# Kernel tuning notes

Measured on AMD Instinct MI355X. Metric: run time of the kernel, lower is better.

The kernel has to match this reference:

```python
import jax, jax.numpy as jnp
import numpy as np

N, E, FEAT, EMB, HID, V, EA, G = 10000, 250000, 16, 32, 32, 12, 9, 64
TEMP = 1.0


def setup_inputs() -> dict:
    key = jax.random.key(0)
    ks = jax.random.split(key, 20)
    p = lambda k, shp: jax.random.normal(k, shp, dtype=jnp.float32) * 0.05
    return {
        "x": jax.random.normal(ks[0], (N, FEAT), dtype=jnp.float32),
        "edge_attr": jax.random.normal(ks[1], (E, EA), dtype=jnp.float32),
        "edge_index": jax.random.randint(ks[2], (2, E), 0, N),
        "batch": jnp.sort(jax.random.randint(ks[3], (N,), 0, G)),
        # conv1 edge MLP: Linear(EA,32) -> ReLU -> Linear(32, FEAT*EMB)
        "nn1_w1": p(ks[4], (EA, 32)), "nn1_b1": p(ks[5], (32,)),
        "nn1_w2": p(ks[6], (32, FEAT * EMB)), "nn1_b2": p(ks[7], (FEAT * EMB,)),
        "root1": p(ks[8], (FEAT, EMB)), "bias1": p(ks[9], (EMB,)),
        # conv2 edge MLP: Linear(EA,32) -> ReLU -> Linear(32, EMB*HID)
        "nn2_w1": p(ks[10], (EA, 32)), "nn2_b1": p(ks[11], (32,)),
        "nn2_w2": p(ks[12], (32, EMB * HID)), "nn2_b2": p(ks[13], (EMB * HID,)),
        "root2": p(ks[14], (EMB, HID)), "bias2": p(ks[15], (HID,)),
        "lin_w": p(ks[16], (HID, V)), "lin_b": p(ks[17], (V,)),
    }


def _segment_mean(vals, ids, num_segments):
    s = jax.ops.segment_sum(vals, ids, num_segments=num_segments)
    cnt = jax.ops.segment_sum(jnp.ones((vals.shape[0],), vals.dtype), ids,
                              num_segments=num_segments)
    return s / jnp.maximum(cnt, 1.0)[:, None]


def _nnconv(h, edge_attr, src, dst, w1, b1, w2, b2, root, bias, din, dout):
    # edge MLP -> per-edge weight matrix [E, din, dout]
    we = (jax.nn.relu(edge_attr @ w1 + b1) @ w2 + b2).reshape(-1, din, dout)
    msg = jnp.einsum('ei,eio->eo', h[src], we)      # gather + per-edge matmul
    agg = _segment_mean(msg, dst, h.shape[0])       # scatter-mean to targets
    return agg + h @ root + bias                    # root weight + bias


def reference(x, edge_attr, edge_index, batch,
              nn1_w1, nn1_b1, nn1_w2, nn1_b2, root1, bias1,
              nn2_w1, nn2_b1, nn2_w2, nn2_b2, root2, bias2,
              lin_w, lin_b):
    src, dst = edge_index[0], edge_index[1]
    h = jax.nn.relu(_nnconv(x, edge_attr, src, dst,
                            nn1_w1, nn1_b1, nn1_w2, nn1_b2, root1, bias1,
                            FEAT, EMB))
    h = jax.nn.relu(_nnconv(h, edge_attr, src, dst,
                            nn2_w1, nn2_b1, nn2_w2, nn2_b2, root2, bias2,
                            EMB, HID))
    pooled = _segment_mean(h, batch, G)             # global_mean_pool [G, HID]
    logits = (pooled @ lin_w + lin_b) / TEMP
    return jax.nn.log_softmax(logits, axis=1)
```

## Files before the change

### kernel.cpp

```cpp
#include <hip/hip_runtime.h>
#include <hip/hip_bf16.h>
#include <stdint.h>

#define NN 10000
#define NE 250000
#define FEAT 16
#define EMB 32
#define HID 32
#define NV 12
#define EAD 9
#define NG 64
#define EPB 128
#define NCH 25

__device__ __forceinline__ uint32_t bf16rne(float f) {
    uint32_t u = __float_as_uint(f);
    return (u + 0x7fffu + ((u >> 16) & 1u)) >> 16;
}
__device__ __forceinline__ float blo(uint32_t p) { return __uint_as_float(p << 16); }
__device__ __forceinline__ float bhi(uint32_t p) { return __uint_as_float(p & 0xffff0000u); }

__global__ void edge_stats_kernel(const int* __restrict__ src,
                                  const int* __restrict__ dst,
                                  int* __restrict__ histS,
                                  int* __restrict__ histD) {
    int e = blockIdx.x * blockDim.x + threadIdx.x;
    if (e >= NE) return;
    atomicAdd(&histS[src[e]], 1);
    atomicAdd(&histD[dst[e]], 1);
}

__global__ __launch_bounds__(1024) void scan_kernel(const int* __restrict__ hist,
                                                    int* __restrict__ rowStart,
                                                    int* __restrict__ cursor) {
    __shared__ int part[1024];
    int t = threadIdx.x;
    int base = t * 10;
    int local[10];
    int s = 0;
#pragma unroll
    for (int i = 0; i < 10; ++i) {
        int v = (base + i < NN) ? hist[base + i] : 0;
        local[i] = s;
        s += v;
    }
    part[t] = s;
    __syncthreads();
    for (int off = 1; off < 1024; off <<= 1) {
        int v = (t >= off) ? part[t - off] : 0;
        __syncthreads();
        part[t] += v;
        __syncthreads();
    }
    int pre = (t == 0) ? 0 : part[t - 1];
#pragma unroll
    for (int i = 0; i < 10; ++i) {
        if (base + i < NN) {
            int rs = pre + local[i];
            rowStart[base + i] = rs;
            cursor[base + i] = rs;
        }
    }
    if (t == 1023) rowStart[NN] = part[1023];
}

__global__ void scatter_kernel(const float* __restrict__ ea,
                               const int* __restrict__ src,
                               const int* __restrict__ dst,
                               int* __restrict__ cursorS,
                               float* __restrict__ ea_p,
                               int* __restrict__ src_s,
                               int* __restrict__ dst_s) {
    int e = blockIdx.x * blockDim.x + threadIdx.x;
    if (e >= NE) return;
    int sv = src[e];
    int pos = atomicAdd(&cursorS[sv], 1);
    src_s[pos] = sv;
    dst_s[pos] = dst[e];
#pragma unroll
    for (int j = 0; j < 12; ++j)
        ea_p[(size_t)pos * 12 + j] = (j < EAD) ? ea[(size_t)e * EAD + j] : 0.f;
}

template <int DIN>
__global__ __launch_bounds__(256) void computeQ_pack_kernel(
    const float* __restrict__ h,
    const float* __restrict__ w2,
    const float* __restrict__ b2,
    uint32_t* __restrict__ Qp,
    float* __restrict__ Qb)
{
    int t = threadIdx.x;
    int o = t & 31;
    int kk = (blockIdx.y * 256 + t) >> 5;
    float w0[DIN], w1r[DIN];
    const float* wa = w2 + (size_t)(2 * kk) * (DIN * 32) + o;
    const float* wb = w2 + (size_t)(2 * kk + 1) * (DIN * 32) + o;
#pragma unroll
    for (int i = 0; i < DIN; ++i) { w0[i] = wa[i * 32]; w1r[i] = wb[i * 32]; }

    int n0 = blockIdx.x * NCH;
    for (int j = 0; j < NCH; ++j) {
        int n = n0 + j;
        const float* hn = h + (size_t)n * DIN;
        float s0 = 0.f, s1 = 0.f;
#pragma unroll
        for (int i = 0; i < DIN; ++i) {
            float hv = hn[i];
            s0 += hv * w0[i];
            s1 += hv * w1r[i];
        }
        Qp[((size_t)n * 16 + kk) * 32 + o] = (bf16rne(s1) << 16) | bf16rne(s0);
        if (kk == 0) {
            float sb = 0.f;
#pragma unroll
            for (int i = 0; i < DIN; ++i) sb += hn[i] * b2[i * 32 + o];
            Qb[(size_t)n * 32 + o] = sb;
        }
    }
}

__global__ __launch_bounds__(256) void edge_agg_kernel(
    const float* __restrict__ ea_p,
    const int* __restrict__ src_s,
    const int* __restrict__ dst_s,
    const float* __restrict__ w1,
    const float* __restrict__ b1,
    const uint32_t* __restrict__ Qp,
    const float* __restrict__ Qb,
    float* __restrict__ agg)
{
    __shared__ float s_hid[8][32];
    int t = threadIdx.x;
    int o = t & 31;
    int slot = t >> 5;

    float w1r[12];
#pragma unroll
    for (int j = 0; j < 12; ++j) w1r[j] = (j < EAD) ? w1[j * 32 + o] : 0.f;
    float b1r = b1[o];

    int base = blockIdx.x * EPB;
    int eend = min(base + EPB, NE);
    for (int e = base + slot; e < eend; e += 8) {
        const float4* eav = (const float4*)(ea_p + (size_t)e * 12);
        float4 a0 = eav[0], a1 = eav[1], a2 = eav[2];
        float hs = b1r;
        hs += a0.x * w1r[0] + a0.y * w1r[1] + a0.z * w1r[2] + a0.w * w1r[3];
        hs += a1.x * w1r[4] + a1.y * w1r[5] + a1.z * w1r[6] + a1.w * w1r[7];
        hs += a2.x * w1r[8];
        float hd = fmaxf(hs, 0.f);

        s_hid[slot][o] = hd;
        __builtin_amdgcn_wave_barrier();

        int sv = src_s[e];
        const uint32_t* q = Qp + (size_t)sv * 512 + o;
        float m = Qb[(size_t)sv * 32 + o];
        const float4* hq = (const float4*)(&s_hid[slot][0]);
#pragma unroll
        for (int c = 0; c < 8; ++c) {
            float4 hv = hq[c];
            uint32_t qa  = q[(2 * c) * 32];
            uint32_t qb2 = q[(2 * c + 1) * 32];
            m += hv.x * blo(qa) + hv.y * bhi(qa)
               + hv.z * blo(qb2) + hv.w * bhi(qb2);
        }
        atomicAdd(&agg[(size_t)dst_s[e] * 32 + o], m);
        __builtin_amdgcn_wave_barrier();
    }
}

template <int DIN>
__global__ __launch_bounds__(256) void node_update_kernel(
    float* __restrict__ agg,
    const int* __restrict__ histD,
    const float* __restrict__ hin,
    const float* __restrict__ root,
    const float* __restrict__ bias,
    float* __restrict__ hout,
    float* __restrict__ pooled,
    const int* __restrict__ batch,
    float* __restrict__ gcnt)
{
    __shared__ float s_root[DIN][32];
    __shared__ float s_h[32][DIN + 1];
    int t = threadIdx.x;
    int n0 = blockIdx.x * 32;

    for (int i = t; i < DIN * 8; i += 256)
        ((float4*)&s_root[0][0])[i] = ((const float4*)root)[i];
    for (int idx = t; idx < 32 * DIN; idx += 256) {
        int nl = idx / DIN, i = idx - nl * DIN;
        int n = n0 + nl;
        s_h[nl][i] = (n < NN) ? hin[(size_t)n * DIN + i] : 0.f;
    }
    __syncthreads();

    int nl = t >> 3;
    int cg = t & 7;
    int n = n0 + nl;
    if (n >= NN) return;

    float inv = 1.0f / fmaxf((float)histD[n], 1.0f);
    float* ap = agg + (size_t)n * 32 + cg * 4;
    float4 a4;
    a4.x = atomicAdd(ap + 0, 0.f);
    a4.y = atomicAdd(ap + 1, 0.f);
    a4.z = atomicAdd(ap + 2, 0.f);
    a4.w = atomicAdd(ap + 3, 0.f);
    *(float4*)ap = make_float4(0.f, 0.f, 0.f, 0.f);

    float4 b4 = *(const float4*)(bias + cg * 4);
    float4 s;
    s.x = a4.x * inv + b4.x;
    s.y = a4.y * inv + b4.y;
    s.z = a4.z * inv + b4.z;
    s.w = a4.w * inv + b4.w;
#pragma unroll
    for (int i = 0; i < DIN; ++i) {
        float hv = s_h[nl][i];
        float4 r4 = *(const float4*)&s_root[i][cg * 4];
        s.x += hv * r4.x; s.y += hv * r4.y; s.z += hv * r4.z; s.w += hv * r4.w;
    }
    s.x = fmaxf(s.x, 0.f); s.y = fmaxf(s.y, 0.f);
    s.z = fmaxf(s.z, 0.f); s.w = fmaxf(s.w, 0.f);
    *(float4*)(hout + (size_t)n * 32 + cg * 4) = s;

    if (pooled) {
        int g = batch[n];
        atomicAdd(&pooled[g * 32 + cg * 4 + 0], s.x);
        atomicAdd(&pooled[g * 32 + cg * 4 + 1], s.y);
        atomicAdd(&pooled[g * 32 + cg * 4 + 2], s.z);
        atomicAdd(&pooled[g * 32 + cg * 4 + 3], s.w);
        if (cg == 0) atomicAdd(&gcnt[g], 1.0f);
    }
}

__global__ void final_kernel(float* __restrict__ pooled,
                             float* __restrict__ gcnt,
                             const float* __restrict__ lin_w,
                             const float* __restrict__ lin_b,
                             float* __restrict__ out) {
    int g = threadIdx.x;
    if (g >= NG) return;
    float inv = 1.0f / fmaxf(atomicAdd(&gcnt[g], 0.f), 1.0f);
    float p[HID];
#pragma unroll
    for (int h = 0; h < HID; ++h) p[h] = atomicAdd(&pooled[g * HID + h], 0.f) * inv;
    float logits[NV];
    float mx = -1e30f;
#pragma unroll
    for (int v = 0; v < NV; ++v) {
        float s = lin_b[v];
#pragma unroll
        for (int h = 0; h < HID; ++h) s += p[h] * lin_w[h * NV + v];
        logits[v] = s;
        mx = fmaxf(mx, s);
    }
    float se = 0.f;
#pragma unroll
    for (int v = 0; v < NV; ++v) se += expf(logits[v] - mx);
    float lse = mx + logf(se);
#pragma unroll
    for (int v = 0; v < NV; ++v) out[g * NV + v] = logits[v] - lse;
}

extern "C" void kernel_launch(void* const* d_in, const int* in_sizes, int n_in,
                              void* d_out, int out_size, void* d_ws, size_t ws_size,
                              hipStream_t stream) {
    const float* x        = (const float*)d_in[0];
    const float* ea       = (const float*)d_in[1];
    const int*   eidx     = (const int*)d_in[2];
    const int*   batch    = (const int*)d_in[3];
    const float* nn1_w1   = (const float*)d_in[4];
    const float* nn1_b1   = (const float*)d_in[5];
    const float* nn1_w2   = (const float*)d_in[6];
    const float* nn1_b2   = (const float*)d_in[7];
    const float* root1    = (const float*)d_in[8];
    const float* bias1    = (const float*)d_in[9];
    const float* nn2_w1   = (const float*)d_in[10];
    const float* nn2_b1   = (const float*)d_in[11];
    const float* nn2_w2   = (const float*)d_in[12];
    const float* nn2_b2   = (const float*)d_in[13];
    const float* root2    = (const float*)d_in[14];
    const float* bias2    = (const float*)d_in[15];
    const float* lin_w    = (const float*)d_in[16];
    const float* lin_b    = (const float*)d_in[17];
    float* out = (float*)d_out;

    const int* src = eidx;
    const int* dst = eidx + NE;

    char* base = (char*)d_ws;
    uint32_t* Qp   = (uint32_t*)base;
    float* ea_p    = (float*)(Qp + (size_t)NN * 512);
    float* Qb      = ea_p + (size_t)NE * 12;
    float* h1      = Qb + (size_t)NN * 32;
    float* h2      = h1 + (size_t)NN * 32;
    float* agg     = h2 + (size_t)NN * 32;
    int*   src_s   = (int*)(agg + (size_t)NN * 32);
    int*   dst_s   = src_s + NE;
    int*   rowS    = dst_s + NE;
    int*   curS    = rowS + NN + 1;
    int*   histS   = curS + NN;
    int*   histD   = histS + NN;
    float* pooled  = (float*)(histD + NN);
    float* gcnt    = pooled + NG * 32;
    size_t zero_bytes = ((size_t)NN * 2 + NG * 32 + NG) * 4;

    hipMemsetAsync(agg, 0, (size_t)NN * 32 * sizeof(float), stream);
    hipMemsetAsync(histS, 0, zero_bytes, stream);

    edge_stats_kernel<<<(NE + 255) / 256, 256, 0, stream>>>(src, dst, histS, histD);
    scan_kernel<<<1, 1024, 0, stream>>>(histS, rowS, curS);
    scatter_kernel<<<(NE + 255) / 256, 256, 0, stream>>>(ea, src, dst, curS,
                                                         ea_p, src_s, dst_s);

    const int edge_grid = (NE + EPB - 1) / EPB;
    const int node_grid = (NN + 31) / 32;
    dim3 qgrid(NN / NCH, 2);

    computeQ_pack_kernel<FEAT><<<qgrid, 256, 0, stream>>>(x, nn1_w2, nn1_b2, Qp, Qb);
    edge_agg_kernel<<<edge_grid, 256, 0, stream>>>(ea_p, src_s, dst_s,
                                                   nn1_w1, nn1_b1, Qp, Qb, agg);
    node_update_kernel<FEAT><<<node_grid, 256, 0, stream>>>(
        agg, histD, x, root1, bias1, h1, nullptr, nullptr, nullptr);

    computeQ_pack_kernel<EMB><<<qgrid, 256, 0, stream>>>(h1, nn2_w2, nn2_b2, Qp, Qb);
    edge_agg_kernel<<<edge_grid, 256, 0, stream>>>(ea_p, src_s, dst_s,
                                                   nn2_w1, nn2_b1, Qp, Qb, agg);
    node_update_kernel<EMB><<<node_grid, 256, 0, stream>>>(
        agg, histD, h1, root2, bias2, h2, pooled, batch, gcnt);

    final_kernel<<<1, 64, 0, stream>>>(pooled, gcnt, lin_w, lin_b, out);
}
```

Baseline: 262.8 us.

## Fuse per-layer kernels into one cooperative persistent kernel with grid syncs

```diff
diff --git a/kernel.cpp b/kernel.cpp
--- a/kernel.cpp
+++ b/kernel.cpp
@@ -1,6 +1,9 @@
 #include <hip/hip_runtime.h>
 #include <hip/hip_bf16.h>
+#include <hip/hip_cooperative_groups.h>
 #include <stdint.h>
+
+namespace cg = cooperative_groups;
 
 #define NN 10000
 #define NE 250000
@@ -82,172 +85,184 @@
         ea_p[(size_t)pos * 12 + j] = (j < EAD) ? ea[(size_t)e * EAD + j] : 0.f;
 }
 
+struct Params {
+    const float* x; const float* ea_p;
+    const int* src_s; const int* dst_s; const int* histD; const int* batch;
+    const float* nn1_w1; const float* nn1_b1; const float* nn1_w2; const float* nn1_b2;
+    const float* root1; const float* bias1;
+    const float* nn2_w1; const float* nn2_b1; const float* nn2_w2; const float* nn2_b2;
+    const float* root2; const float* bias2;
+    const float* lin_w; const float* lin_b;
+    uint32_t* Qp; float* Qb; float* agg; float* h1; float* h2;
+    float* pooled; float* gcnt; float* out;
+};
+
 template <int DIN>
-__global__ __launch_bounds__(256) void computeQ_pack_kernel(
-    const float* __restrict__ h,
-    const float* __restrict__ w2,
-    const float* __restrict__ b2,
-    uint32_t* __restrict__ Qp,
-    float* __restrict__ Qb)
-{
+__device__ void computeQ_phase(const float* __restrict__ h,
+                               const float* __restrict__ w2,
+                               const float* __restrict__ b2,
+                               uint32_t* __restrict__ Qp,
+                               float* __restrict__ Qb,
+                               float* smem) {
     int t = threadIdx.x;
     int o = t & 31;
-    int kk = (blockIdx.y * 256 + t) >> 5;
-    float w0[DIN], w1r[DIN];
-    const float* wa = w2 + (size_t)(2 * kk) * (DIN * 32) + o;
-    const float* wb = w2 + (size_t)(2 * kk + 1) * (DIN * 32) + o;
-#pragma unroll
-    for (int i = 0; i < DIN; ++i) { w0[i] = wa[i * 32]; w1r[i] = wb[i * 32]; }
-
-    int n0 = blockIdx.x * NCH;
-    for (int j = 0; j < NCH; ++j) {
-        int n = n0 + j;
-        const float* hn = h + (size_t)n * DIN;
-        float s0 = 0.f, s1 = 0.f;
-#pragma unroll
-        for (int i = 0; i < DIN; ++i) {
-            float hv = hn[i];
-            s0 += hv * w0[i];
-            s1 += hv * w1r[i];
-        }
-        Qp[((size_t)n * 16 + kk) * 32 + o] = (bf16rne(s1) << 16) | bf16rne(s0);
-        if (kk == 0) {
-            float sb = 0.f;
-#pragma unroll
-            for (int i = 0; i < DIN; ++i) sb += hn[i] * b2[i * 32 + o];
-            Qb[(size_t)n * 32 + o] = sb;
-        }
-    }
-}
-
-__global__ __launch_bounds__(256) void edge_agg_kernel(
-    const float* __restrict__ ea_p,
-    const int* __restrict__ src_s,
-    const int* __restrict__ dst_s,
-    const float* __restrict__ w1,
-    const float* __restrict__ b1,
-    const uint32_t* __restrict__ Qp,
-    const float* __restrict__ Qb,
-    float* __restrict__ agg)
-{
-    __shared__ float s_hid[8][32];
+    const int NVB = (NN / NCH) * 2;
+    for (int vb = blockIdx.x; vb < NVB; vb += gridDim.x) {
+        int nb = vb >> 1;
+        int kk = (vb & 1) * 8 + (t >> 5);
+        int n0 = nb * NCH;
+        __syncthreads();
+        for (int idx = t; idx < NCH * DIN; idx += 256)
+            smem[idx] = h[(size_t)n0 * DIN + idx];
+        __syncthreads();
+        float w0[DIN], w1r[DIN];
+        const float* wa = w2 + (size_t)(2 * kk) * (DIN * 32) + o;
+        const float* wb = w2 + (size_t)(2 * kk + 1) * (DIN * 32) + o;
+#pragma unroll
+        for (int i = 0; i < DIN; ++i) { w0[i] = wa[i * 32]; w1r[i] = wb[i * 32]; }
+        for (int j = 0; j < NCH; ++j) {
+            const float* sh = smem + j * DIN;
+            float s0 = 0.f, s1 = 0.f;
+#pragma unroll
+            for (int i4 = 0; i4 < DIN / 4; ++i4) {
+                float4 hv = *(const float4*)(sh + i4 * 4);
+                s0 += hv.x * w0[4*i4] + hv.y * w0[4*i4+1] + hv.z * w0[4*i4+2] + hv.w * w0[4*i4+3];
+                s1 += hv.x * w1r[4*i4] + hv.y * w1r[4*i4+1] + hv.z * w1r[4*i4+2] + hv.w * w1r[4*i4+3];
+            }
+            int n = n0 + j;
+            Qp[((size_t)n * 16 + kk) * 32 + o] = (bf16rne(s1) << 16) | bf16rne(s0);
+            if (kk == 0) {
+                float sb = 0.f;
+#pragma unroll
+                for (int i = 0; i < DIN; ++i) sb += sh[i] * b2[i * 32 + o];
+                Qb[(size_t)n * 32 + o] = sb;
+            }
+        }
+    }
+}
+
+__device__ void edge_phase(const float* __restrict__ ea_p,
+                           const int* __restrict__ src_s,
+                           const int* __restrict__ dst_s,
+                           const float* __restrict__ w1,
+                           const float* __restrict__ b1,
+                           const uint32_t* __restrict__ Qp,
+                           const float* __restrict__ Qb,
+                           float* __restrict__ agg,
+                           float* smem) {
+    float* s_hid = smem;
     int t = threadIdx.x;
     int o = t & 31;
     int slot = t >> 5;
-
-    float w1r[12];
-#pragma unroll
-    for (int j = 0; j < 12; ++j) w1r[j] = (j < EAD) ? w1[j * 32 + o] : 0.f;
+    float w1r[EAD];
+#pragma unroll
+    for (int j = 0; j < EAD; ++j) w1r[j] = w1[j * 32 + o];
     float b1r = b1[o];
 
-    int base = blockIdx.x * EPB;
-    int eend = min(base + EPB, NE);
-    for (int e = base + slot; e < eend; e += 8) {
-        const float4* eav = (const float4*)(ea_p + (size_t)e * 12);
-        float4 a0 = eav[0], a1 = eav[1], a2 = eav[2];
-        float hs = b1r;
-        hs += a0.x * w1r[0] + a0.y * w1r[1] + a0.z * w1r[2] + a0.w * w1r[3];
-        hs += a1.x * w1r[4] + a1.y * w1r[5] + a1.z * w1r[6] + a1.w * w1r[7];
-        hs += a2.x * w1r[8];
-        float hd = fmaxf(hs, 0.f);
-
-        s_hid[slot][o] = hd;
-        __builtin_amdgcn_wave_barrier();
-
-        int sv = src_s[e];
-        const uint32_t* q = Qp + (size_t)sv * 512 + o;
-        float m = Qb[(size_t)sv * 32 + o];
-        const float4* hq = (const float4*)(&s_hid[slot][0]);
-#pragma unroll
-        for (int c = 0; c < 8; ++c) {
-            float4 hv = hq[c];
-            uint32_t qa  = q[(2 * c) * 32];
-            uint32_t qb2 = q[(2 * c + 1) * 32];
-            m += hv.x * blo(qa) + hv.y * bhi(qa)
-               + hv.z * blo(qb2) + hv.w * bhi(qb2);
-        }
-        atomicAdd(&agg[(size_t)dst_s[e] * 32 + o], m);
-        __builtin_amdgcn_wave_barrier();
-    }
-}
-
-template <int DIN>
-__global__ __launch_bounds__(256) void node_update_kernel(
-    float* __restrict__ agg,
-    const int* __restrict__ histD,
-    const float* __restrict__ hin,
-    const float* __restrict__ root,
-    const float* __restrict__ bias,
-    float* __restrict__ hout,
-    float* __restrict__ pooled,
-    const int* __restrict__ batch,
-    float* __restrict__ gcnt)
-{
-    __shared__ float s_root[DIN][32];
-    __shared__ float s_h[32][DIN + 1];
+    const int NCHK = (NE + EPB - 1) / EPB;
+    for (int vb = blockIdx.x; vb < NCHK; vb += gridDim.x) {
+        int base = vb * EPB, eend = min(base + EPB, NE);
+        for (int e = base + slot; e < eend; e += 8) {
+            const float4* eav = (const float4*)(ea_p + (size_t)e * 12);
+            float4 a0 = eav[0], a1 = eav[1], a2 = eav[2];
+            float hs = b1r;
+            hs += a0.x * w1r[0] + a0.y * w1r[1] + a0.z * w1r[2] + a0.w * w1r[3];
+            hs += a1.x * w1r[4] + a1.y * w1r[5] + a1.z * w1r[6] + a1.w * w1r[7];
+            hs += a2.x * w1r[8];
+            float hd = fmaxf(hs, 0.f);
+
+            s_hid[slot * 32 + o] = hd;
+            __builtin_amdgcn_wave_barrier();
+
+            int sv = src_s[e];
+            const uint32_t* q = Qp + (size_t)sv * 512 + o;
+            float m = Qb[(size_t)sv * 32 + o];
+            const float4* hq = (const float4*)(s_hid + slot * 32);
+#pragma unroll
+            for (int c = 0; c < 8; ++c) {
+                float4 hv = hq[c];
+                uint32_t qa  = q[(2 * c) * 32];
+                uint32_t qb2 = q[(2 * c + 1) * 32];
+                m += hv.x * blo(qa) + hv.y * bhi(qa)
+                   + hv.z * blo(qb2) + hv.w * bhi(qb2);
+            }
+            atomicAdd(&agg[(size_t)dst_s[e] * 32 + o], m);
+            __builtin_amdgcn_wave_barrier();
+        }
+    }
+}
+
+template <int DIN, bool POOL>
+__device__ void node_phase(float* __restrict__ agg,
+                           const int* __restrict__ histD,
+                           const float* __restrict__ hin,
+                           const float* __restrict__ root,
+                           const float* __restrict__ bias,
+                           float* __restrict__ hout,
+                           float* __restrict__ pooled,
+                           const int* __restrict__ batch,
+                           float* __restrict__ gcnt,
+                           float* smem) {
+    float* s_root = smem;
+    float* s_h    = smem + DIN * 32;
     int t = threadIdx.x;
-    int n0 = blockIdx.x * 32;
-
-    for (int i = t; i < DIN * 8; i += 256)
-        ((float4*)&s_root[0][0])[i] = ((const float4*)root)[i];
-    for (int idx = t; idx < 32 * DIN; idx += 256) {
-        int nl = idx / DIN, i = idx - nl * DIN;
+    const int NVB = (NN + 31) / 32;
+    for (int vb = blockIdx.x; vb < NVB; vb += gridDim.x) {
+        int n0 = vb * 32;
+        __syncthreads();
+        for (int i = t; i < DIN * 8; i += 256)
+            ((float4*)s_root)[i] = ((const float4*)root)[i];
+        for (int idx = t; idx < 32 * DIN; idx += 256) {
+            int nl = idx / DIN, i = idx - nl * DIN;
+            int n = n0 + nl;
+            s_h[nl * (DIN + 1) + i] = (n < NN) ? hin[(size_t)n * DIN + i] : 0.f;
+        }
+        __syncthreads();
+        int nl = t >> 3, cg4 = t & 7;
         int n = n0 + nl;
-        s_h[nl][i] = (n < NN) ? hin[(size_t)n * DIN + i] : 0.f;
-    }
-    __syncthreads();
-
-    int nl = t >> 3;
-    int cg = t & 7;
-    int n = n0 + nl;
-    if (n >= NN) return;
-
-    float inv = 1.0f / fmaxf((float)histD[n], 1.0f);
-    float* ap = agg + (size_t)n * 32 + cg * 4;
-    float4 a4;
-    a4.x = atomicAdd(ap + 0, 0.f);
-    a4.y = atomicAdd(ap + 1, 0.f);
-    a4.z = atomicAdd(ap + 2, 0.f);
-    a4.w = atomicAdd(ap + 3, 0.f);
-    *(float4*)ap = make_float4(0.f, 0.f, 0.f, 0.f);
-
-    float4 b4 = *(const float4*)(bias + cg * 4);
-    float4 s;
-    s.x = a4.x * inv + b4.x;
-    s.y = a4.y * inv + b4.y;
-    s.z = a4.z * inv + b4.z;
-    s.w = a4.w * inv + b4.w;
-#pragma unroll
-    for (int i = 0; i < DIN; ++i) {
-        float hv = s_h[nl][i];
-        float4 r4 = *(const float4*)&s_root[i][cg * 4];
-        s.x += hv * r4.x; s.y += hv * r4.y; s.z += hv * r4.z; s.w += hv * r4.w;
-    }
-    s.x = fmaxf(s.x, 0.f); s.y = fmaxf(s.y, 0.f);
-    s.z = fmaxf(s.z, 0.f); s.w = fmaxf(s.w, 0.f);
-    *(float4*)(hout + (size_t)n * 32 + cg * 4) = s;
-
-    if (pooled) {
-        int g = batch[n];
-        atomicAdd(&pooled[g * 32 + cg * 4 + 0], s.x);
-        atomicAdd(&pooled[g * 32 + cg * 4 + 1], s.y);
-        atomicAdd(&pooled[g * 32 + cg * 4 + 2], s.z);
-        atomicAdd(&pooled[g * 32 + cg * 4 + 3], s.w);
-        if (cg == 0) atomicAdd(&gcnt[g], 1.0f);
-    }
-}
-
-__global__ void final_kernel(float* __restrict__ pooled,
-                             float* __restrict__ gcnt,
-                             const float* __restrict__ lin_w,
-                             const float* __restrict__ lin_b,
-                             float* __restrict__ out) {
+        if (n < NN) {
+            float inv = 1.0f / fmaxf((float)histD[n], 1.0f);
+            float* ap = agg + (size_t)n * 32 + cg4 * 4;
+            float4 a4 = *(const float4*)ap;
+            *(float4*)ap = make_float4(0.f, 0.f, 0.f, 0.f);
+            float4 b4 = *(const float4*)(bias + cg4 * 4);
+            float4 s;
+            s.x = a4.x * inv + b4.x;
+            s.y = a4.y * inv + b4.y;
+            s.z = a4.z * inv + b4.z;
+            s.w = a4.w * inv + b4.w;
+#pragma unroll
+            for (int i = 0; i < DIN; ++i) {
+                float hv = s_h[nl * (DIN + 1) + i];
+                float4 r4 = *(const float4*)(s_root + i * 32 + cg4 * 4);
+                s.x += hv * r4.x; s.y += hv * r4.y; s.z += hv * r4.z; s.w += hv * r4.w;
+            }
+            s.x = fmaxf(s.x, 0.f); s.y = fmaxf(s.y, 0.f);
+            s.z = fmaxf(s.z, 0.f); s.w = fmaxf(s.w, 0.f);
+            *(float4*)(hout + (size_t)n * 32 + cg4 * 4) = s;
+            if (POOL) {
+                int g = batch[n];
+                atomicAdd(&pooled[g * 32 + cg4 * 4 + 0], s.x);
+                atomicAdd(&pooled[g * 32 + cg4 * 4 + 1], s.y);
+                atomicAdd(&pooled[g * 32 + cg4 * 4 + 2], s.z);
+                atomicAdd(&pooled[g * 32 + cg4 * 4 + 3], s.w);
+                if (cg4 == 0) atomicAdd(&gcnt[g], 1.0f);
+            }
+        }
+    }
+}
+
+__device__ void final_phase(const float* __restrict__ pooled,
+                            const float* __restrict__ gcnt,
+                            const float* __restrict__ lin_w,
+                            const float* __restrict__ lin_b,
+                            float* __restrict__ out) {
     int g = threadIdx.x;
     if (g >= NG) return;
-    float inv = 1.0f / fmaxf(atomicAdd(&gcnt[g], 0.f), 1.0f);
+    float inv = 1.0f / fmaxf(gcnt[g], 1.0f);
     float p[HID];
 #pragma unroll
-    for (int h = 0; h < HID; ++h) p[h] = atomicAdd(&pooled[g * HID + h], 0.f) * inv;
+    for (int h = 0; h < HID; ++h) p[h] = pooled[g * HID + h] * inv;
     float logits[NV];
     float mx = -1e30f;
 #pragma unroll
@@ -266,28 +281,49 @@
     for (int v = 0; v < NV; ++v) out[g * NV + v] = logits[v] - lse;
 }
 
+__global__ __launch_bounds__(256) void mega_kernel(Params P) {
+    __shared__ __align__(16) float smem[2080];
+    cg::grid_group grid = cg::this_grid();
+
+    computeQ_phase<FEAT>(P.x, P.nn1_w2, P.nn1_b2, P.Qp, P.Qb, smem);
+    grid.sync();
+    edge_phase(P.ea_p, P.src_s, P.dst_s, P.nn1_w1, P.nn1_b1, P.Qp, P.Qb, P.agg, smem);
+    grid.sync();
+    node_phase<FEAT, false>(P.agg, P.histD, P.x, P.root1, P.bias1, P.h1,
+                            nullptr, nullptr, nullptr, smem);
+    grid.sync();
+    computeQ_phase<EMB>(P.h1, P.nn2_w2, P.nn2_b2, P.Qp, P.Qb, smem);
+    grid.sync();
+    edge_phase(P.ea_p, P.src_s, P.dst_s, P.nn2_w1, P.nn2_b1, P.Qp, P.Qb, P.agg, smem);
+    grid.sync();
+    node_phase<EMB, true>(P.agg, P.histD, P.h1, P.root2, P.bias2, P.h2,
+                          P.pooled, P.batch, P.gcnt, smem);
+    grid.sync();
+    if (blockIdx.x == 0) final_phase(P.pooled, P.gcnt, P.lin_w, P.lin_b, P.out);
+}
+
+__global__ __launch_bounds__(256) void phase_kernel(Params P, int ph) {
+    __shared__ __align__(16) float smem[2080];
+    switch (ph) {
+    case 0: computeQ_phase<FEAT>(P.x, P.nn1_w2, P.nn1_b2, P.Qp, P.Qb, smem); break;
+    case 1: edge_phase(P.ea_p, P.src_s, P.dst_s, P.nn1_w1, P.nn1_b1, P.Qp, P.Qb, P.agg, smem); break;
+    case 2: node_phase<FEAT, false>(P.agg, P.histD, P.x, P.root1, P.bias1, P.h1,
+                                    nullptr, nullptr, nullptr, smem); break;
+    case 3: computeQ_phase<EMB>(P.h1, P.nn2_w2, P.nn2_b2, P.Qp, P.Qb, smem); break;
+    case 4: edge_phase(P.ea_p, P.src_s, P.dst_s, P.nn2_w1, P.nn2_b1, P.Qp, P.Qb, P.agg, smem); break;
+    case 5: node_phase<EMB, true>(P.agg, P.histD, P.h1, P.root2, P.bias2, P.h2,
+                                  P.pooled, P.batch, P.gcnt, smem); break;
+    case 6: if (blockIdx.x == 0) final_phase(P.pooled, P.gcnt, P.lin_w, P.lin_b, P.out); break;
+    }
+}
+
 extern "C" void kernel_launch(void* const* d_in, const int* in_sizes, int n_in,
                               void* d_out, int out_size, void* d_ws, size_t ws_size,
                               hipStream_t stream) {
-    const float* x        = (const float*)d_in[0];
-    const float* ea       = (const float*)d_in[1];
-    const int*   eidx     = (const int*)d_in[2];
-    const int*   batch    = (const int*)d_in[3];
-    const float* nn1_w1   = (const float*)d_in[4];
-    const float* nn1_b1   = (const float*)d_in[5];
-    const float* nn1_w2   = (const float*)d_in[6];
-    const float* nn1_b2   = (const float*)d_in[7];
-    const float* root1    = (const float*)d_in[8];
-    const float* bias1    = (const float*)d_in[9];
-    const float* nn2_w1   = (const float*)d_in[10];
-    const float* nn2_b1   = (const float*)d_in[11];
-    const float* nn2_w2   = (const float*)d_in[12];
-    const float* nn2_b2   = (const float*)d_in[13];
-    const float* root2    = (const float*)d_in[14];
-    const float* bias2    = (const float*)d_in[15];
-    const float* lin_w    = (const float*)d_in[16];
-    const float* lin_b    = (const float*)d_in[17];
-    float* out = (float*)d_out;
+    const float* x      = (const float*)d_in[0];
+    const float* ea     = (const float*)d_in[1];
+    const int*   eidx   = (const int*)d_in[2];
+    const int*   batch  = (const int*)d_in[3];
 
     const int* src = eidx;
     const int* dst = eidx + NE;
@@ -317,21 +353,37 @@
     scatter_kernel<<<(NE + 255) / 256, 256, 0, stream>>>(ea, src, dst, curS,
                                                          ea_p, src_s, dst_s);
 
-    const int edge_grid = (NE + EPB - 1) / EPB;
-    const int node_grid = (NN + 31) / 32;
-    dim3 qgrid(NN / NCH, 2);
-
-    computeQ_pack_kernel<FEAT><<<qgrid, 256, 0, stream>>>(x, nn1_w2, nn1_b2, Qp, Qb);
-    edge_agg_kernel<<<edge_grid, 256, 0, stream>>>(ea_p, src_s, dst_s,
-                                                   nn1_w1, nn1_b1, Qp, Qb, agg);
-    node_update_kernel<FEAT><<<node_grid, 256, 0, stream>>>(
-        agg, histD, x, root1, bias1, h1, nullptr, nullptr, nullptr);
-
-    computeQ_pack_kernel<EMB><<<qgrid, 256, 0, stream>>>(h1, nn2_w2, nn2_b2, Qp, Qb);
-    edge_agg_kernel<<<edge_grid, 256, 0, stream>>>(ea_p, src_s, dst_s,
-                                                   nn2_w1, nn2_b1, Qp, Qb, agg);
-    node_update_kernel<EMB><<<node_grid, 256, 0, stream>>>(
-        agg, histD, h1, root2, bias2, h2, pooled, batch, gcnt);
-
-    final_kernel<<<1, 64, 0, stream>>>(pooled, gcnt, lin_w, lin_b, out);
-}
+    Params P;
+    P.x = x; P.ea_p = ea_p; P.src_s = src_s; P.dst_s = dst_s;
+    P.histD = histD; P.batch = batch;
+    P.nn1_w1 = (const float*)d_in[4];  P.nn1_b1 = (const float*)d_in[5];
+    P.nn1_w2 = (const float*)d_in[6];  P.nn1_b2 = (const float*)d_in[7];
+    P.root1  = (const float*)d_in[8];  P.bias1  = (const float*)d_in[9];
+    P.nn2_w1 = (const float*)d_in[10]; P.nn2_b1 = (const float*)d_in[11];
+    P.nn2_w2 = (const float*)d_in[12]; P.nn2_b2 = (const float*)d_in[13];
+    P.root2  = (const float*)d_in[14]; P.bias2  = (const float*)d_in[15];
+    P.lin_w  = (const float*)d_in[16]; P.lin_b  = (const float*)d_in[17];
+    P.Qp = Qp; P.Qb = Qb; P.agg = agg; P.h1 = h1; P.h2 = h2;
+    P.pooled = pooled; P.gcnt = gcnt; P.out = (float*)d_out;
+
+    int maxBlocksPerCU = 0;
+    hipError_t qerr = hipOccupancyMaxActiveBlocksPerMultiprocessor(
+        &maxBlocksPerCU, mega_kernel, 256, 0);
+    int cus = 0;
+    hipDeviceGetAttribute(&cus, hipDeviceAttributeMultiprocessorCount, 0);
+    int grid = (qerr == hipSuccess && maxBlocksPerCU > 0 && cus > 0)
+                   ? maxBlocksPerCU * cus : 0;
+    if (grid > 2048) grid = 2048;
+
+    hipError_t lerr = hipErrorUnknown;
+    if (grid > 0) {
+        void* kp[] = { (void*)&P };
+        lerr = hipLaunchCooperativeKernel(mega_kernel, dim3(grid), dim3(256),
+                                          kp, 0, stream);
+    }
+    if (lerr != hipSuccess) {
+        int g2 = 1024;
+        for (int ph = 0; ph < 7; ++ph)
+            phase_kernel<<<g2, 256, 0, stream>>>(P, ph);
+    }
+}
```

Result: slower. 584.8 us (+122.6%).

## Use packed bf16 atomics for aggregation and precompute layer-2 edge hidden

Applied to the files above, without the earlier changes.

```diff
diff --git a/kernel.cpp b/kernel.cpp
--- a/kernel.cpp
+++ b/kernel.cpp
@@ -19,6 +19,11 @@
 }
 __device__ __forceinline__ float blo(uint32_t p) { return __uint_as_float(p << 16); }
 __device__ __forceinline__ float bhi(uint32_t p) { return __uint_as_float(p & 0xffff0000u); }
+
+__device__ __forceinline__ void atomic_pk_add_bf16(uint32_t* addr, uint32_t packed) {
+    asm volatile("global_atomic_pk_add_bf16 %0, %1, off"
+                 :: "v"((uint64_t)(uintptr_t)addr), "v"(packed) : "memory");
+}
 
 __global__ void edge_stats_kernel(const int* __restrict__ src,
                                   const int* __restrict__ dst,
@@ -120,60 +125,112 @@
     }
 }
 
+__global__ __launch_bounds__(256) void hidden_kernel(
+    const float* __restrict__ ea_p,
+    const float* __restrict__ w1,
+    const float* __restrict__ b1,
+    uint2* __restrict__ hid2)
+{
+    int t = threadIdx.x;
+    int e = blockIdx.x * 32 + (t >> 3);
+    int c = t & 7;
+    if (e >= NE) return;
+    const float4* eav = (const float4*)(ea_p + (size_t)e * 12);
+    float4 a0 = eav[0], a1 = eav[1], a2 = eav[2];
+    float hv[4];
+#pragma unroll
+    for (int kk = 0; kk < 4; ++kk) {
+        int o = 4 * c + kk;
+        float hs = b1[o];
+        hs += a0.x * w1[0 * 32 + o] + a0.y * w1[1 * 32 + o]
+            + a0.z * w1[2 * 32 + o] + a0.w * w1[3 * 32 + o];
+        hs += a1.x * w1[4 * 32 + o] + a1.y * w1[5 * 32 + o]
+            + a1.z * w1[6 * 32 + o] + a1.w * w1[7 * 32 + o];
+        hs += a2.x * w1[8 * 32 + o];
+        hv[kk] = fmaxf(hs, 0.f);
+    }
+    uint2 p;
+    p.x = (bf16rne(hv[1]) << 16) | bf16rne(hv[0]);
+    p.y = (bf16rne(hv[3]) << 16) | bf16rne(hv[2]);
+    hid2[(size_t)e * 8 + c] = p;
+}
+
+template <bool PRE>
 __global__ __launch_bounds__(256) void edge_agg_kernel(
     const float* __restrict__ ea_p,
+    const uint2* __restrict__ hid2,
     const int* __restrict__ src_s,
     const int* __restrict__ dst_s,
     const float* __restrict__ w1,
     const float* __restrict__ b1,
     const uint32_t* __restrict__ Qp,
     const float* __restrict__ Qb,
-    float* __restrict__ agg)
+    uint32_t* __restrict__ aggbf)
 {
     __shared__ float s_hid[8][32];
     int t = threadIdx.x;
     int o = t & 31;
     int slot = t >> 5;
 
-    float w1r[12];
-#pragma unroll
-    for (int j = 0; j < 12; ++j) w1r[j] = (j < EAD) ? w1[j * 32 + o] : 0.f;
-    float b1r = b1[o];
+    float w1r[EAD];
+    float b1r = 0.f;
+    if (!PRE) {
+#pragma unroll
+        for (int j = 0; j < EAD; ++j) w1r[j] = w1[j * 32 + o];
+        b1r = b1[o];
+    }
 
     int base = blockIdx.x * EPB;
     int eend = min(base + EPB, NE);
     for (int e = base + slot; e < eend; e += 8) {
-        const float4* eav = (const float4*)(ea_p + (size_t)e * 12);
-        float4 a0 = eav[0], a1 = eav[1], a2 = eav[2];
-        float hs = b1r;
-        hs += a0.x * w1r[0] + a0.y * w1r[1] + a0.z * w1r[2] + a0.w * w1r[3];
-        hs += a1.x * w1r[4] + a1.y * w1r[5] + a1.z * w1r[6] + a1.w * w1r[7];
-        hs += a2.x * w1r[8];
-        float hd = fmaxf(hs, 0.f);
-
-        s_hid[slot][o] = hd;
-        __builtin_amdgcn_wave_barrier();
+        if (!PRE) {
+            const float4* eav = (const float4*)(ea_p + (size_t)e * 12);
+            float4 a0 = eav[0], a1 = eav[1], a2 = eav[2];
+            float hs = b1r;
+            hs += a0.x * w1r[0] + a0.y * w1r[1] + a0.z * w1r[2] + a0.w * w1r[3];
+            hs += a1.x * w1r[4] + a1.y * w1r[5] + a1.z * w1r[6] + a1.w * w1r[7];
+            hs += a2.x * w1r[8];
+            s_hid[slot][o] = fmaxf(hs, 0.f);
+            __builtin_amdgcn_wave_barrier();
+        }
 
         int sv = src_s[e];
         const uint32_t* q = Qp + (size_t)sv * 512 + o;
         float m = Qb[(size_t)sv * 32 + o];
-        const float4* hq = (const float4*)(&s_hid[slot][0]);
-#pragma unroll
-        for (int c = 0; c < 8; ++c) {
-            float4 hv = hq[c];
-            uint32_t qa  = q[(2 * c) * 32];
-            uint32_t qb2 = q[(2 * c + 1) * 32];
-            m += hv.x * blo(qa) + hv.y * bhi(qa)
-               + hv.z * blo(qb2) + hv.w * bhi(qb2);
-        }
-        atomicAdd(&agg[(size_t)dst_s[e] * 32 + o], m);
-        __builtin_amdgcn_wave_barrier();
-    }
-}
-
-template <int DIN>
+        if (PRE) {
+            const uint2* hp2 = hid2 + (size_t)e * 8;
+#pragma unroll
+            for (int c = 0; c < 8; ++c) {
+                uint2 hp = hp2[c];
+                uint32_t qa  = q[(2 * c) * 32];
+                uint32_t qb2 = q[(2 * c + 1) * 32];
+                m += blo(hp.x) * blo(qa) + bhi(hp.x) * bhi(qa)
+                   + blo(hp.y) * blo(qb2) + bhi(hp.y) * bhi(qb2);
+            }
+        } else {
+            const float4* hq = (const float4*)(&s_hid[slot][0]);
+#pragma unroll
+            for (int c = 0; c < 8; ++c) {
+                float4 hv = hq[c];
+                uint32_t qa  = q[(2 * c) * 32];
+                uint32_t qb2 = q[(2 * c + 1) * 32];
+                m += hv.x * blo(qa) + hv.y * bhi(qa)
+                   + hv.z * blo(qb2) + hv.w * bhi(qb2);
+            }
+        }
+
+        float m1 = __shfl_down(m, 1, 32);
+        if (!(o & 1)) {
+            uint32_t packed = (bf16rne(m1) << 16) | bf16rne(m);
+            atomic_pk_add_bf16(aggbf + (size_t)dst_s[e] * 16 + (o >> 1), packed);
+        }
+        if (!PRE) __builtin_amdgcn_wave_barrier();
+    }
+}
+
+template <int DIN, bool POOL>
 __global__ __launch_bounds__(256) void node_update_kernel(
-    float* __restrict__ agg,
+    uint32_t* __restrict__ aggbf,
     const int* __restrict__ histD,
     const float* __restrict__ hin,
     const float* __restrict__ root,
@@ -203,20 +260,16 @@
     if (n >= NN) return;
 
     float inv = 1.0f / fmaxf((float)histD[n], 1.0f);
-    float* ap = agg + (size_t)n * 32 + cg * 4;
-    float4 a4;
-    a4.x = atomicAdd(ap + 0, 0.f);
-    a4.y = atomicAdd(ap + 1, 0.f);
-    a4.z = atomicAdd(ap + 2, 0.f);
-    a4.w = atomicAdd(ap + 3, 0.f);
-    *(float4*)ap = make_float4(0.f, 0.f, 0.f, 0.f);
+    uint2* ap = (uint2*)(aggbf + (size_t)n * 16 + cg * 2);
+    uint2 a2 = *ap;
+    *ap = make_uint2(0u, 0u);
 
     float4 b4 = *(const float4*)(bias + cg * 4);
     float4 s;
-    s.x = a4.x * inv + b4.x;
-    s.y = a4.y * inv + b4.y;
-    s.z = a4.z * inv + b4.z;
-    s.w = a4.w * inv + b4.w;
+    s.x = blo(a2.x) * inv + b4.x;
+    s.y = bhi(a2.x) * inv + b4.y;
+    s.z = blo(a2.y) * inv + b4.z;
+    s.w = bhi(a2.y) * inv + b4.w;
 #pragma unroll
     for (int i = 0; i < DIN; ++i) {
         float hv = s_h[nl][i];
@@ -227,7 +280,7 @@
     s.z = fmaxf(s.z, 0.f); s.w = fmaxf(s.w, 0.f);
     *(float4*)(hout + (size_t)n * 32 + cg * 4) = s;
 
-    if (pooled) {
+    if (POOL) {
         int g = batch[n];
         atomicAdd(&pooled[g * 32 + cg * 4 + 0], s.x);
         atomicAdd(&pooled[g * 32 + cg * 4 + 1], s.y);
@@ -237,17 +290,17 @@
     }
 }
 
-__global__ void final_kernel(float* __restrict__ pooled,
-                             float* __restrict__ gcnt,
+__global__ void final_kernel(const float* __restrict__ pooled,
+                             const float* __restrict__ gcnt,
                              const float* __restrict__ lin_w,
                              const float* __restrict__ lin_b,
                              float* __restrict__ out) {
     int g = threadIdx.x;
     if (g >= NG) return;
-    float inv = 1.0f / fmaxf(atomicAdd(&gcnt[g], 0.f), 1.0f);
+    float inv = 1.0f / fmaxf(gcnt[g], 1.0f);
     float p[HID];
 #pragma unroll
-    for (int h = 0; h < HID; ++h) p[h] = atomicAdd(&pooled[g * HID + h], 0.f) * inv;
+    for (int h = 0; h < HID; ++h) p[h] = pooled[g * HID + h] * inv;
     float logits[NV];
     float mx = -1e30f;
 #pragma unroll
@@ -293,23 +346,24 @@
     const int* dst = eidx + NE;
 
     char* base = (char*)d_ws;
-    uint32_t* Qp   = (uint32_t*)base;
-    float* ea_p    = (float*)(Qp + (size_t)NN * 512);
-    float* Qb      = ea_p + (size_t)NE * 12;
-    float* h1      = Qb + (size_t)NN * 32;
-    float* h2      = h1 + (size_t)NN * 32;
-    float* agg     = h2 + (size_t)NN * 32;
-    int*   src_s   = (int*)(agg + (size_t)NN * 32);
-    int*   dst_s   = src_s + NE;
-    int*   rowS    = dst_s + NE;
-    int*   curS    = rowS + NN + 1;
-    int*   histS   = curS + NN;
-    int*   histD   = histS + NN;
-    float* pooled  = (float*)(histD + NN);
-    float* gcnt    = pooled + NG * 32;
+    uint32_t* Qp    = (uint32_t*)base;
+    float* ea_p     = (float*)(Qp + (size_t)NN * 512);
+    uint2* hid2     = (uint2*)(ea_p + (size_t)NE * 12);
+    float* Qb       = (float*)(hid2 + (size_t)NE * 8);
+    float* h1       = Qb + (size_t)NN * 32;
+    float* h2       = h1 + (size_t)NN * 32;
+    uint32_t* aggbf = (uint32_t*)(h2 + (size_t)NN * 32);
+    int*   src_s    = (int*)(aggbf + (size_t)NN * 16);
+    int*   dst_s    = src_s + NE;
+    int*   rowS     = dst_s + NE;
+    int*   curS     = rowS + NN + 1;
+    int*   histS    = curS + NN;
+    int*   histD    = histS + NN;
+    float* pooled   = (float*)(histD + NN);
+    float* gcnt     = pooled + NG * 32;
     size_t zero_bytes = ((size_t)NN * 2 + NG * 32 + NG) * 4;
 
-    hipMemsetAsync(agg, 0, (size_t)NN * 32 * sizeof(float), stream);
+    hipMemsetAsync(aggbf, 0, (size_t)NN * 16 * 4, stream);
     hipMemsetAsync(histS, 0, zero_bytes, stream);
 
     edge_stats_kernel<<<(NE + 255) / 256, 256, 0, stream>>>(src, dst, histS, histD);
@@ -319,19 +373,21 @@
 
     const int edge_grid = (NE + EPB - 1) / EPB;
     const int node_grid = (NN + 31) / 32;
+    const int hid_grid  = (NE + 31) / 32;
     dim3 qgrid(NN / NCH, 2);
 
     computeQ_pack_kernel<FEAT><<<qgrid, 256, 0, stream>>>(x, nn1_w2, nn1_b2, Qp, Qb);
-    edge_agg_kernel<<<edge_grid, 256, 0, stream>>>(ea_p, src_s, dst_s,
-                                                   nn1_w1, nn1_b1, Qp, Qb, agg);
-    node_update_kernel<FEAT><<<node_grid, 256, 0, stream>>>(
-        agg, histD, x, root1, bias1, h1, nullptr, nullptr, nullptr);
+    edge_agg_kernel<false><<<edge_grid, 256, 0, stream>>>(
+        ea_p, nullptr, src_s, dst_s, nn1_w1, nn1_b1, Qp, Qb, aggbf);
+    hidden_kernel<<<hid_grid, 256, 0, stream>>>(ea_p, nn2_w1, nn2_b1, hid2);
+    node_update_kernel<FEAT, false><<<node_grid, 256, 0, stream>>>(
+        aggbf, histD, x, root1, bias1, h1, nullptr, nullptr, nullptr);
 
     computeQ_pack_kernel<EMB><<<qgrid, 256, 0, stream>>>(h1, nn2_w2, nn2_b2, Qp, Qb);
-    edge_agg_kernel<<<edge_grid, 256, 0, stream>>>(ea_p, src_s, dst_s,
-                                                   nn2_w1, nn2_b1, Qp, Qb, agg);
-    node_update_kernel<EMB><<<node_grid, 256, 0, stream>>>(
-        agg, histD, h1, root2, bias2, h2, pooled, batch, gcnt);
+    edge_agg_kernel<true><<<edge_grid, 256, 0, stream>>>(
+        ea_p, hid2, src_s, dst_s, nn2_w1, nn2_b1, Qp, Qb, aggbf);
+    node_update_kernel<EMB, true><<<node_grid, 256, 0, stream>>>(
+        aggbf, histD, h1, root2, bias2, h2, pooled, batch, gcnt);
 
     final_kernel<<<1, 64, 0, stream>>>(pooled, gcnt, lin_w, lin_b, out);
 }
```

Result: slower. 271.8 us (+3.4%).
